# Kernel optimization log

Hardware: AMD Instinct MI355X
Metric: run time of the kernel (lower is better)

## Reference

```python
import jax, jax.numpy as jnp
import numpy as np

N_USERS = 4096
N_ITEMS = 4096
D = 64
L = 2
B = 4096
N = N_USERS + N_ITEMS


def setup_inputs() -> dict:
    key = jax.random.key(0)
    ks = jax.random.split(key, 24)
    g = lambda i, shape: jax.random.normal(ks[i], shape, dtype=jnp.float32) * 0.05
    # sparse-ish 0/1 adjacency (module calls adj.to_dense(); ~16 neighbors/node)
    adj = (jax.random.uniform(ks[0], (N, N), dtype=jnp.float32) < 0.002).astype(jnp.float32)
    users = jax.random.randint(ks[1], (B,), 0, N_USERS)
    pos_items = jax.random.randint(ks[2], (B,), 0, N_ITEMS)
    neg_items = jax.random.randint(ks[3], (B,), 0, N_ITEMS)
    return {
        "adj_matrix": adj,
        "users": users,
        "pos_items": pos_items,
        "neg_items": neg_items,
        "user_table": g(4, (N_USERS, D)),
        "item_table": g(5, (N_ITEMS, D)),
        "gcn_W": g(6, (L, D, D)), "gcn_b": g(7, (L, D)),
        "gat_W": g(8, (L, D, D)), "gat_b": g(9, (L, D)),
        "attn_W": g(10, (L, 2 * D)), "attn_b": g(11, (L,)),
        "fuse_W": g(12, (L, 2 * D, D)), "fuse_b": g(13, (L, D)),
        "actor_W": g(14, (D, D)), "actor_b": g(15, (D,)),
        "critic_W1": g(16, (2 * D, D)), "critic_b1": g(17, (D,)),
        "critic_W2": g(18, (D, 1)), "critic_b2": g(19, (1,)),
        "layer_weights": jnp.ones((L,), dtype=jnp.float32),
    }


def _leaky(x):
    return jnp.where(x >= 0, x, 0.01 * x)  # F.leaky_relu default slope


def reference(adj_matrix, users, pos_items, neg_items, user_table, item_table,
              gcn_W, gcn_b, gat_W, gat_b, attn_W, attn_b, fuse_W, fuse_b,
              actor_W, actor_b, critic_W1, critic_b1, critic_W2, critic_b2,
              layer_weights):
    all_emb = jnp.concatenate([user_table, item_table], axis=0)  # [N, D]

    # GCN stack: spmm(adj, x) then linear, relu
    gcn = [all_emb]
    for l in range(L):
        h = adj_matrix @ gcn[-1]
        gcn.append(jax.nn.relu(h @ gcn_W[l] + gcn_b[l]))

    # GAT stack: e[i,j] = leaky_relu(a1.h_i + a2.h_j + b); multiply-mask by adj, row softmax
    gat = [all_emb]
    for l in range(L):
        h = gat[-1] @ gat_W[l] + gat_b[l]  # [N, D]
        a1, a2 = attn_W[l, :D], attn_W[l, D:]
        e = _leaky((h @ a1)[:, None] + (h @ a2)[None, :] + attn_b[l])  # [N, N]
        attn = jax.nn.softmax(e * adj_matrix, axis=1)  # faithful: multiply-mask, not -inf
        gat.append(jax.nn.relu(attn @ h))

    lw = jax.nn.softmax(layer_weights)
    fused = jnp.zeros((N, D), dtype=all_emb.dtype)
    for i in range(L):
        cat = jnp.concatenate([gcn[i + 1], gat[i + 1]], axis=1)  # [N, 2D]
        fused = fused + lw[i] * jax.nn.relu(cat @ fuse_W[i] + fuse_b[i])

    user_emb, item_emb = fused[:N_USERS], fused[N_USERS:]
    u = user_emb[users]
    p = item_emb[pos_items]
    n = item_emb[neg_items]

    uf = u @ actor_W + actor_b  # Actor
    pos_score = jnp.sum(uf * p, axis=1)
    neg_score = jnp.sum(uf * n, axis=1)

    def critic(a, b):
        x = jnp.concatenate([a, b], axis=1)
        hidden = jax.nn.relu(x @ critic_W1 + critic_b1)
        return hidden @ critic_W2 + critic_b2

    return pos_score, neg_score, critic(u, p), critic(u, n)
```

## Files before the change

kernel.cpp:

```cpp
#include <hip/hip_runtime.h>

#define NTOT 8192
#define NU 4096
#define D 64
#define MAXN 128

__device__ __forceinline__ float wave_sum(float x){
  #pragma unroll
  for(int off=32;off;off>>=1) x += __shfl_xor(x,off);
  return x;
}
__device__ __forceinline__ float wave_max(float x){
  #pragma unroll
  for(int off=32;off;off>>=1) x = fmaxf(x,__shfl_xor(x,off));
  return x;
}

__global__ __launch_bounds__(256) void build_ell(const float* __restrict__ adj,
                                                 int* __restrict__ ell,
                                                 int* __restrict__ nnz){
  int lane = threadIdx.x & 63;
  int row  = blockIdx.x * 4 + (threadIdx.x >> 6);
  const float4* arow = (const float4*)(adj + (size_t)row * NTOT);
  int base = 0;
  for(int c0 = 0; c0 < NTOT/4; c0 += 64){
    float4 v = arow[c0 + lane];
    #pragma unroll
    for(int j = 0; j < 4; ++j){
      float f = (j==0)?v.x:(j==1)?v.y:(j==2)?v.z:v.w;
      unsigned long long m = __ballot(f != 0.0f);
      if(f != 0.0f){
        int slot = base + __popcll(m & ((1ull<<lane)-1ull));
        if(slot < MAXN) ell[row*MAXN + slot] = (c0 + lane)*4 + j;
      }
      base += __popcll(m);
    }
  }
  if(lane == 0) nnz[row] = base > MAXN ? MAXN : base;
}

__global__ void concat_emb(const float* __restrict__ ut, const float* __restrict__ it,
                           float* __restrict__ all_emb){
  int i = blockIdx.x * 256 + threadIdx.x;
  all_emb[i] = (i < NU*D) ? ut[i] : it[i - NU*D];
}

__global__ __launch_bounds__(256) void gcn_layer(const float* __restrict__ x,
    const int* __restrict__ ell, const int* __restrict__ nnz,
    const float* __restrict__ W, const float* __restrict__ b,
    float* __restrict__ y){
  __shared__ float Ws[D*D];
  __shared__ float bs[D];
  for(int i = threadIdx.x; i < D*D; i += 256) Ws[i] = W[i];
  if(threadIdx.x < D) bs[threadIdx.x] = b[threadIdx.x];
  __syncthreads();
  int lane = threadIdx.x & 63;
  int row  = blockIdx.x * 4 + (threadIdx.x >> 6);
  int cnt  = nnz[row];
  const int* cols = ell + row*MAXN;
  float acc = 0.f;
  for(int t = 0; t < cnt; ++t){
    int j = cols[t];
    acc += x[j*D + lane];
  }
  float yd = bs[lane];
  #pragma unroll 8
  for(int k = 0; k < D; ++k) yd += __shfl(acc, k) * Ws[k*D + lane];
  y[row*D + lane] = fmaxf(yd, 0.f);
}

__global__ __launch_bounds__(256) void gat_h(const float* __restrict__ x,
    const float* __restrict__ W, const float* __restrict__ b,
    const float* __restrict__ aW,
    float* __restrict__ h, float* __restrict__ qv, float* __restrict__ kvv){
  __shared__ float Ws[D*D];
  __shared__ float bs[D], a1s[D], a2s[D];
  for(int i = threadIdx.x; i < D*D; i += 256) Ws[i] = W[i];
  if(threadIdx.x < D){
    bs[threadIdx.x]  = b[threadIdx.x];
    a1s[threadIdx.x] = aW[threadIdx.x];
    a2s[threadIdx.x] = aW[D + threadIdx.x];
  }
  __syncthreads();
  int lane = threadIdx.x & 63;
  int row  = blockIdx.x * 4 + (threadIdx.x >> 6);
  float xd = x[row*D + lane];
  float hd = bs[lane];
  #pragma unroll 8
  for(int k = 0; k < D; ++k) hd += __shfl(xd, k) * Ws[k*D + lane];
  h[row*D + lane] = hd;
  float q  = wave_sum(hd * a1s[lane]);
  float kk = wave_sum(hd * a2s[lane]);
  if(lane == 0){ qv[row] = q; kvv[row] = kk; }
}

__global__ void colsum_part(const float* __restrict__ h, float* __restrict__ part){
  int d = threadIdx.x;
  int b = blockIdx.x;
  float s = 0.f;
  for(int r = b*32; r < b*32 + 32; ++r) s += h[r*D + d];
  part[b*D + d] = s;
}
__global__ void colsum_final(const float* __restrict__ part, float* __restrict__ S){
  int d = threadIdx.x;
  float s = 0.f;
  for(int b = 0; b < 256; ++b) s += part[b*D + d];
  S[d] = s;
}

__global__ __launch_bounds__(256) void gat_attn(const float* __restrict__ h,
    const float* __restrict__ qv, const float* __restrict__ kvv,
    const int* __restrict__ ell, const int* __restrict__ nnz,
    const float* __restrict__ S, const float* __restrict__ attn_b_p,
    float* __restrict__ out){
  int lane = threadIdx.x & 63;
  int row  = blockIdx.x * 4 + (threadIdx.x >> 6);
  int cnt  = nnz[row];
  float q  = qv[row];
  float ab = attn_b_p[0];
  const int* cols = ell + row*MAXN;
  float m = 0.f;
  for(int t0 = 0; t0 < cnt; t0 += 64){
    int t = t0 + lane;
    float e = -1e30f;
    if(t < cnt){
      float x = q + kvv[cols[t]] + ab;
      e = (x >= 0.f) ? x : 0.01f * x;
    }
    m = fmaxf(m, wave_max(e));
  }
  float em = expf(-m);
  float Z  = (float)(NTOT - cnt) * em;
  float accd = 0.f, hsumd = 0.f;
  for(int t0 = 0; t0 < cnt; t0 += 64){
    int t = t0 + lane;
    float w = 0.f; int col = 0;
    if(t < cnt){
      col = cols[t];
      float x = q + kvv[col] + ab;
      float e = (x >= 0.f) ? x : 0.01f * x;
      w = expf(e - m);
    }
    Z += wave_sum(w);
    int lim = (cnt - t0 < 64) ? (cnt - t0) : 64;
    for(int tt = 0; tt < lim; ++tt){
      float wt = __shfl(w, tt);
      int  j   = __shfl(col, tt);
      float hv = h[j*D + lane];
      accd  += wt * hv;
      hsumd += hv;
    }
  }
  float outd = (accd + em * (S[lane] - hsumd)) / Z;
  out[row*D + lane] = fmaxf(outd, 0.f);
}

__global__ __launch_bounds__(256) void fuse_kernel(const float* __restrict__ gcn1,
    const float* __restrict__ gat1, const float* __restrict__ gcn2, const float* __restrict__ gat2,
    const float* __restrict__ fuse_W, const float* __restrict__ fuse_b,
    const float* __restrict__ layer_w, float* __restrict__ fused){
  __shared__ float Wf[2*D*D];
  __shared__ float bf_[D];
  int lane = threadIdx.x & 63;
  int row  = blockIdx.x * 4 + (threadIdx.x >> 6);
  float l0 = layer_w[0], l1 = layer_w[1];
  float mx = fmaxf(l0, l1);
  float e0 = expf(l0-mx), e1 = expf(l1-mx);
  float inv = 1.f/(e0+e1);
  float lw0 = e0*inv, lw1 = e1*inv;

  for(int i = threadIdx.x; i < 2*D*D; i += 256) Wf[i] = fuse_W[i];
  if(threadIdx.x < D) bf_[threadIdx.x] = fuse_b[threadIdx.x];
  __syncthreads();
  float g = gcn1[row*D + lane], a = gat1[row*D + lane];
  float y0 = bf_[lane];
  #pragma unroll 8
  for(int k = 0; k < D; ++k){
    y0 += __shfl(g, k) * Wf[k*D + lane];
    y0 += __shfl(a, k) * Wf[(D+k)*D + lane];
  }
  __syncthreads();
  for(int i = threadIdx.x; i < 2*D*D; i += 256) Wf[i] = fuse_W[2*D*D + i];
  if(threadIdx.x < D) bf_[threadIdx.x] = fuse_b[D + threadIdx.x];
  __syncthreads();
  g = gcn2[row*D + lane]; a = gat2[row*D + lane];
  float y1 = bf_[lane];
  #pragma unroll 8
  for(int k = 0; k < D; ++k){
    y1 += __shfl(g, k) * Wf[k*D + lane];
    y1 += __shfl(a, k) * Wf[(D+k)*D + lane];
  }
  fused[row*D + lane] = lw0*fmaxf(y0,0.f) + lw1*fmaxf(y1,0.f);
}

__global__ __launch_bounds__(256) void score_kernel(const float* __restrict__ fused,
    const int* __restrict__ users, const int* __restrict__ pos, const int* __restrict__ neg,
    const float* __restrict__ AW, const float* __restrict__ abias,
    const float* __restrict__ cW1, const float* __restrict__ cb1,
    const float* __restrict__ cW2, const float* __restrict__ cb2,
    float* __restrict__ out){
  __shared__ float AWs[D*D];
  __shared__ float C1s[2*D*D];
  __shared__ float abs_[D], cb1s[D], C2s[D];
  for(int i = threadIdx.x; i < D*D; i += 256) AWs[i] = AW[i];
  for(int i = threadIdx.x; i < 2*D*D; i += 256) C1s[i] = cW1[i];
  if(threadIdx.x < D){
    abs_[threadIdx.x] = abias[threadIdx.x];
    cb1s[threadIdx.x] = cb1[threadIdx.x];
    C2s[threadIdx.x]  = cW2[threadIdx.x];
  }
  __syncthreads();
  int lane = threadIdx.x & 63;
  int bi   = blockIdx.x * 4 + (threadIdx.x >> 6);
  int ui = users[bi], pi = pos[bi] + NU, ni = neg[bi] + NU;
  float ud = fused[ui*D + lane], pd = fused[pi*D + lane], nd = fused[ni*D + lane];
  float ufd = abs_[lane];
  #pragma unroll 8
  for(int k = 0; k < D; ++k) ufd += __shfl(ud, k) * AWs[k*D + lane];
  float ps = wave_sum(ufd * pd);
  float ns = wave_sum(ufd * nd);
  float hu = cb1s[lane];
  #pragma unroll 8
  for(int k = 0; k < D; ++k) hu += __shfl(ud, k) * C1s[k*D + lane];
  float hp = hu, hn = hu;
  #pragma unroll 8
  for(int k = 0; k < D; ++k){
    float pk = __shfl(pd, k), nk = __shfl(nd, k);
    hp += pk * C1s[(D+k)*D + lane];
    hn += nk * C1s[(D+k)*D + lane];
  }
  hp = fmaxf(hp, 0.f); hn = fmaxf(hn, 0.f);
  float cp = wave_sum(hp * C2s[lane]);
  float cn = wave_sum(hn * C2s[lane]);
  if(lane == 0){
    out[bi]          = ps;
    out[4096  + bi]  = ns;
    out[8192  + bi]  = cp + cb2[0];
    out[12288 + bi]  = cn + cb2[0];
  }
}

extern "C" void kernel_launch(void* const* d_in, const int* in_sizes, int n_in,
                              void* d_out, int out_size, void* d_ws, size_t ws_size,
                              hipStream_t stream){
  const float* adj        = (const float*)d_in[0];
  const int*   users      = (const int*)d_in[1];
  const int*   pos        = (const int*)d_in[2];
  const int*   neg        = (const int*)d_in[3];
  const float* user_table = (const float*)d_in[4];
  const float* item_table = (const float*)d_in[5];
  const float* gcn_W      = (const float*)d_in[6];
  const float* gcn_b      = (const float*)d_in[7];
  const float* gat_W      = (const float*)d_in[8];
  const float* gat_b      = (const float*)d_in[9];
  const float* attn_W     = (const float*)d_in[10];
  const float* attn_b     = (const float*)d_in[11];
  const float* fuse_W     = (const float*)d_in[12];
  const float* fuse_b     = (const float*)d_in[13];
  const float* actor_W    = (const float*)d_in[14];
  const float* actor_b    = (const float*)d_in[15];
  const float* cW1        = (const float*)d_in[16];
  const float* cb1        = (const float*)d_in[17];
  const float* cW2        = (const float*)d_in[18];
  const float* cb2        = (const float*)d_in[19];
  const float* layer_w    = (const float*)d_in[20];

  const int ND = NTOT * D;
  float* ws      = (float*)d_ws;
  float* all_emb = ws;
  float* gcn1    = all_emb + ND;
  float* gcn2    = gcn1 + ND;
  float* gat1    = gcn2 + ND;
  float* gat2    = gat1 + ND;
  float* hbuf    = gat2 + ND;
  float* fusedb  = hbuf + ND;
  float* qv      = fusedb + ND;
  float* kv      = qv + NTOT;
  float* Spart   = kv + NTOT;
  float* Svec    = Spart + 256*D;
  int*   nnz     = (int*)(Svec + D);
  int*   ell     = nnz + NTOT;

  build_ell<<<NTOT/4, 256, 0, stream>>>(adj, ell, nnz);
  concat_emb<<<ND/256, 256, 0, stream>>>(user_table, item_table, all_emb);

  gcn_layer<<<NTOT/4, 256, 0, stream>>>(all_emb, ell, nnz, gcn_W,        gcn_b,     gcn1);
  gcn_layer<<<NTOT/4, 256, 0, stream>>>(gcn1,    ell, nnz, gcn_W + D*D,  gcn_b + D, gcn2);

  gat_h<<<NTOT/4, 256, 0, stream>>>(all_emb, gat_W, gat_b, attn_W, hbuf, qv, kv);
  colsum_part<<<256, 64, 0, stream>>>(hbuf, Spart);
  colsum_final<<<1, 64, 0, stream>>>(Spart, Svec);
  gat_attn<<<NTOT/4, 256, 0, stream>>>(hbuf, qv, kv, ell, nnz, Svec, attn_b, gat1);

  gat_h<<<NTOT/4, 256, 0, stream>>>(gat1, gat_W + D*D, gat_b + D, attn_W + 2*D, hbuf, qv, kv);
  colsum_part<<<256, 64, 0, stream>>>(hbuf, Spart);
  colsum_final<<<1, 64, 0, stream>>>(Spart, Svec);
  gat_attn<<<NTOT/4, 256, 0, stream>>>(hbuf, qv, kv, ell, nnz, Svec, attn_b + 1, gat2);

  fuse_kernel<<<NTOT/4, 256, 0, stream>>>(gcn1, gat1, gcn2, gat2, fuse_W, fuse_b, layer_w, fusedb);
  score_kernel<<<4096/4, 256, 0, stream>>>(fusedb, users, pos, neg,
                                           actor_W, actor_b, cW1, cb1, cW2, cb2,
                                           (float*)d_out);
}
```

Before: 210.0 us.

## Fuse pipeline into five multi-role kernels with padded ELL and atomic column sums

Replaces the roughly fourteen launches with five kernels. Independent stages share one launch by splitting the grid on block index: ELL build with concat, GCN layer with GAT projection, and GCN layer 2 with GAT attention 1, the first fuse half and the GAT layer 2 projection. The two-pass column sum becomes per-block atomicAdds. The ELL width drops to 64 and is padded with a sentinel index that points at a zero row, so gathers can be unrolled by 8 without bounds checks. Shuffles are replaced with readlane broadcasts, and all-zero float4 chunks are skipped in the adjacency scan. The gains come from fewer launches and sync points, and the cost is a dependence on every row having at most 64 neighbours, plus float atomic ordering nondeterminism.

Measured after the change: 221.1 us. 5.3% more time.

```diff
diff --git a/kernel.cpp b/kernel.cpp
--- a/kernel.cpp
+++ b/kernel.cpp
@@ -1,199 +1,256 @@
 #include <hip/hip_runtime.h>
 
 #define NTOT 8192
+#define NROW 2048
 #define NU 4096
 #define D 64
-#define MAXN 128
-
-__device__ __forceinline__ float wave_sum(float x){
+#define MAXN 64
+#define ND (NTOT*D)
+
+__device__ __forceinline__ float wsum(float x){
   #pragma unroll
-  for(int off=32;off;off>>=1) x += __shfl_xor(x,off);
+  for(int o=32;o;o>>=1) x += __shfl_xor(x,o);
   return x;
 }
-__device__ __forceinline__ float wave_max(float x){
+__device__ __forceinline__ float wmax(float x){
   #pragma unroll
-  for(int off=32;off;off>>=1) x = fmaxf(x,__shfl_xor(x,off));
+  for(int o=32;o;o>>=1) x = fmaxf(x,__shfl_xor(x,o));
   return x;
 }
-
-__global__ __launch_bounds__(256) void build_ell(const float* __restrict__ adj,
-                                                 int* __restrict__ ell,
-                                                 int* __restrict__ nnz){
-  int lane = threadIdx.x & 63;
-  int row  = blockIdx.x * 4 + (threadIdx.x >> 6);
-  const float4* arow = (const float4*)(adj + (size_t)row * NTOT);
-  int base = 0;
-  for(int c0 = 0; c0 < NTOT/4; c0 += 64){
-    float4 v = arow[c0 + lane];
-    #pragma unroll
-    for(int j = 0; j < 4; ++j){
-      float f = (j==0)?v.x:(j==1)?v.y:(j==2)?v.z:v.w;
-      unsigned long long m = __ballot(f != 0.0f);
-      if(f != 0.0f){
-        int slot = base + __popcll(m & ((1ull<<lane)-1ull));
-        if(slot < MAXN) ell[row*MAXN + slot] = (c0 + lane)*4 + j;
+__device__ __forceinline__ float bcastf(float x, int k){
+  return __uint_as_float(__builtin_amdgcn_readlane(__float_as_uint(x), (unsigned)k));
+}
+__device__ __forceinline__ int bcasti(int x, int k){
+  return (int)__builtin_amdgcn_readlane((unsigned)x, (unsigned)k);
+}
+
+__device__ __forceinline__ float gat_attn_row(const float* __restrict__ h,
+    const float* __restrict__ kvv, const float* __restrict__ S,
+    const int* __restrict__ cols, int cnt, float q, float ab, int lane){
+  int t = lane;
+  int col = (t < cnt) ? cols[t] : 0;
+  float e = -1e30f;
+  if(t < cnt){
+    float xx = q + kvv[col] + ab;
+    e = (xx >= 0.f) ? xx : 0.01f * xx;
+  }
+  float m  = fmaxf(0.f, wmax(e));
+  float w  = (t < cnt) ? expf(e - m) : 0.f;
+  float em = expf(-m);
+  float Z  = (float)(NTOT - cnt) * em + wsum(w);
+  float acc = 0.f, hsum = 0.f;
+  for(int tt = 0; tt < cnt; ++tt){
+    float wt = bcastf(w, tt);
+    int   jc = bcasti(col, tt);
+    float hv = h[jc*D + lane];
+    acc  = fmaf(wt, hv, acc);
+    hsum += hv;
+  }
+  float outv = (acc + em * (S[lane] - hsum)) / Z;
+  return fmaxf(outv, 0.f);
+}
+
+__global__ __launch_bounds__(256) void kA(const float* __restrict__ adj,
+    const float* __restrict__ ut, const float* __restrict__ it,
+    float* __restrict__ all_emb, int* __restrict__ ell, int* __restrict__ nnz,
+    float* __restrict__ Svec0, float* __restrict__ Svec1, float* __restrict__ gcn1){
+  int bid = blockIdx.x, tid = threadIdx.x;
+  if(bid < NROW){
+    int lane = tid & 63;
+    int row  = bid*4 + (tid >> 6);
+    ell[row*MAXN + lane] = NTOT;
+    const float4* arow = (const float4*)(adj + (size_t)row * NTOT);
+    int base = 0;
+    for(int c0 = 0; c0 < NTOT/4; c0 += 64){
+      float4 v = arow[c0 + lane];
+      int nib = (v.x!=0.f?1:0) | (v.y!=0.f?2:0) | (v.z!=0.f?4:0) | (v.w!=0.f?8:0);
+      if(__ballot(nib != 0) == 0ull) continue;
+      #pragma unroll
+      for(int j = 0; j < 4; ++j){
+        unsigned long long m = __ballot(((nib>>j)&1) != 0);
+        if(m){
+          if((nib>>j)&1){
+            int below = __builtin_amdgcn_mbcnt_hi((unsigned)(m>>32),
+                        __builtin_amdgcn_mbcnt_lo((unsigned)m, 0u));
+            int slot = base + below;
+            if(slot < MAXN) ell[row*MAXN + slot] = (c0 + lane)*4 + j;
+          }
+          base += __popcll(m);
+        }
       }
-      base += __popcll(m);
-    }
-  }
-  if(lane == 0) nnz[row] = base > MAXN ? MAXN : base;
-}
-
-__global__ void concat_emb(const float* __restrict__ ut, const float* __restrict__ it,
-                           float* __restrict__ all_emb){
-  int i = blockIdx.x * 256 + threadIdx.x;
-  all_emb[i] = (i < NU*D) ? ut[i] : it[i - NU*D];
-}
-
-__global__ __launch_bounds__(256) void gcn_layer(const float* __restrict__ x,
+    }
+    if(lane == 0) nnz[row] = base > MAXN ? MAXN : base;
+  } else if(bid < 2*NROW){
+    int i = (bid - NROW)*256 + tid;
+    all_emb[i] = (i < NU*D) ? ut[i] : it[i - NU*D];
+  } else {
+    if(tid < D){
+      Svec0[tid] = 0.f; Svec1[tid] = 0.f;
+      all_emb[ND + tid] = 0.f;
+      gcn1[ND + tid]    = 0.f;
+    }
+  }
+}
+
+__global__ __launch_bounds__(256) void kB(const float* __restrict__ all_emb,
     const int* __restrict__ ell, const int* __restrict__ nnz,
-    const float* __restrict__ W, const float* __restrict__ b,
-    float* __restrict__ y){
+    const float* __restrict__ gcn_W, const float* __restrict__ gcn_b,
+    const float* __restrict__ gat_W, const float* __restrict__ gat_b,
+    const float* __restrict__ attn_W,
+    float* __restrict__ gcn1, float* __restrict__ h0,
+    float* __restrict__ qv0, float* __restrict__ kv0, float* __restrict__ Svec0){
   __shared__ float Ws[D*D];
-  __shared__ float bs[D];
-  for(int i = threadIdx.x; i < D*D; i += 256) Ws[i] = W[i];
-  if(threadIdx.x < D) bs[threadIdx.x] = b[threadIdx.x];
-  __syncthreads();
-  int lane = threadIdx.x & 63;
-  int row  = blockIdx.x * 4 + (threadIdx.x >> 6);
-  int cnt  = nnz[row];
+  __shared__ float red[4][D];
+  int tid = threadIdx.x, lane = tid & 63, wid = tid >> 6;
+  int bid = blockIdx.x;
+  if(bid < NROW){
+    for(int i = tid; i < D*D; i += 256) Ws[i] = gcn_W[i];
+    __syncthreads();
+    int row = bid*4 + wid;
+    int cnt = nnz[row];
+    const int* cols = ell + row*MAXN;
+    float acc = 0.f;
+    int cnt8 = (cnt + 7) & ~7;
+    for(int t = 0; t < cnt8; t += 8){
+      #pragma unroll
+      for(int u = 0; u < 8; ++u){
+        int j = cols[t + u];
+        acc += all_emb[j*D + lane];
+      }
+    }
+    float y = gcn_b[lane];
+    #pragma unroll 16
+    for(int k = 0; k < D; ++k) y = fmaf(bcastf(acc, k), Ws[k*D + lane], y);
+    gcn1[row*D + lane] = fmaxf(y, 0.f);
+  } else {
+    for(int i = tid; i < D*D; i += 256) Ws[i] = gat_W[i];
+    __syncthreads();
+    int row = (bid - NROW)*4 + wid;
+    float xr = all_emb[row*D + lane];
+    float h = gat_b[lane];
+    #pragma unroll 16
+    for(int k = 0; k < D; ++k) h = fmaf(bcastf(xr, k), Ws[k*D + lane], h);
+    h0[row*D + lane] = h;
+    float q  = wsum(h * attn_W[lane]);
+    float kk = wsum(h * attn_W[D + lane]);
+    if(lane == 0){ qv0[row] = q; kv0[row] = kk; }
+    red[wid][lane] = h;
+    __syncthreads();
+    if(wid == 0){
+      float s = red[0][lane] + red[1][lane] + red[2][lane] + red[3][lane];
+      atomicAdd(&Svec0[lane], s);
+    }
+  }
+}
+
+__global__ __launch_bounds__(256) void kC(
+    const float* __restrict__ all_emb, const int* __restrict__ ell, const int* __restrict__ nnz,
+    const float* __restrict__ gcn1, const float* __restrict__ h0,
+    const float* __restrict__ qv0, const float* __restrict__ kv0, const float* __restrict__ Svec0,
+    const float* __restrict__ gcn_W, const float* __restrict__ gcn_b,
+    const float* __restrict__ gat_W, const float* __restrict__ gat_b,
+    const float* __restrict__ attn_W, const float* __restrict__ attn_b,
+    const float* __restrict__ fuse_W, const float* __restrict__ fuse_b,
+    const float* __restrict__ layer_w,
+    float* __restrict__ gcn2, float* __restrict__ h1,
+    float* __restrict__ qv1, float* __restrict__ kv1, float* __restrict__ Svec1,
+    float* __restrict__ fusedb){
+  __shared__ float Ws[D*D];
+  __shared__ float red[4][D];
+  int tid = threadIdx.x, lane = tid & 63, wid = tid >> 6;
+  int bid = blockIdx.x;
+  if(bid < NROW){
+    for(int i = tid; i < D*D; i += 256) Ws[i] = gcn_W[D*D + i];
+    __syncthreads();
+    int row = bid*4 + wid;
+    int cnt = nnz[row];
+    const int* cols = ell + row*MAXN;
+    float acc = 0.f;
+    int cnt8 = (cnt + 7) & ~7;
+    for(int t = 0; t < cnt8; t += 8){
+      #pragma unroll
+      for(int u = 0; u < 8; ++u){
+        int j = cols[t + u];
+        acc += gcn1[j*D + lane];
+      }
+    }
+    float y = gcn_b[D + lane];
+    #pragma unroll 16
+    for(int k = 0; k < D; ++k) y = fmaf(bcastf(acc, k), Ws[k*D + lane], y);
+    gcn2[row*D + lane] = fmaxf(y, 0.f);
+  } else {
+    int row = (bid - NROW)*4 + wid;
+    int cnt = nnz[row];
+    const int* cols = ell + row*MAXN;
+    float g1 = gat_attn_row(h0, kv0, Svec0, cols, cnt, qv0[row], attn_b[0], lane);
+    float gc1 = gcn1[row*D + lane];
+    float l0 = layer_w[0], l1 = layer_w[1];
+    float mx = fmaxf(l0, l1);
+    float e0 = expf(l0 - mx), e1 = expf(l1 - mx);
+    float lw0 = e0 / (e0 + e1);
+    for(int i = tid; i < D*D; i += 256) Ws[i] = fuse_W[i];
+    __syncthreads();
+    float y = fuse_b[lane];
+    #pragma unroll 16
+    for(int k = 0; k < D; ++k) y = fmaf(bcastf(gc1, k), Ws[k*D + lane], y);
+    __syncthreads();
+    for(int i = tid; i < D*D; i += 256) Ws[i] = fuse_W[D*D + i];
+    __syncthreads();
+    #pragma unroll 16
+    for(int k = 0; k < D; ++k) y = fmaf(bcastf(g1, k), Ws[k*D + lane], y);
+    fusedb[row*D + lane] = lw0 * fmaxf(y, 0.f);
+    __syncthreads();
+    for(int i = tid; i < D*D; i += 256) Ws[i] = gat_W[D*D + i];
+    __syncthreads();
+    float h = gat_b[D + lane];
+    #pragma unroll 16
+    for(int k = 0; k < D; ++k) h = fmaf(bcastf(g1, k), Ws[k*D + lane], h);
+    h1[row*D + lane] = h;
+    float qq = wsum(h * attn_W[2*D + lane]);
+    float kk = wsum(h * attn_W[3*D + lane]);
+    if(lane == 0){ qv1[row] = qq; kv1[row] = kk; }
+    red[wid][lane] = h;
+    __syncthreads();
+    if(wid == 0){
+      float s = red[0][lane] + red[1][lane] + red[2][lane] + red[3][lane];
+      atomicAdd(&Svec1[lane], s);
+    }
+  }
+}
+
+__global__ __launch_bounds__(256) void kE(
+    const int* __restrict__ ell, const int* __restrict__ nnz,
+    const float* __restrict__ gcn2, const float* __restrict__ h1,
+    const float* __restrict__ qv1, const float* __restrict__ kv1, const float* __restrict__ Svec1,
+    const float* __restrict__ attn_b,
+    const float* __restrict__ fuse_W, const float* __restrict__ fuse_b,
+    const float* __restrict__ layer_w,
+    float* __restrict__ fusedb){
+  __shared__ float Ws[D*D];
+  int tid = threadIdx.x, lane = tid & 63, wid = tid >> 6;
+  int row = blockIdx.x*4 + wid;
+  int cnt = nnz[row];
   const int* cols = ell + row*MAXN;
-  float acc = 0.f;
-  for(int t = 0; t < cnt; ++t){
-    int j = cols[t];
-    acc += x[j*D + lane];
-  }
-  float yd = bs[lane];
-  #pragma unroll 8
-  for(int k = 0; k < D; ++k) yd += __shfl(acc, k) * Ws[k*D + lane];
-  y[row*D + lane] = fmaxf(yd, 0.f);
-}
-
-__global__ __launch_bounds__(256) void gat_h(const float* __restrict__ x,
-    const float* __restrict__ W, const float* __restrict__ b,
-    const float* __restrict__ aW,
-    float* __restrict__ h, float* __restrict__ qv, float* __restrict__ kvv){
-  __shared__ float Ws[D*D];
-  __shared__ float bs[D], a1s[D], a2s[D];
-  for(int i = threadIdx.x; i < D*D; i += 256) Ws[i] = W[i];
-  if(threadIdx.x < D){
-    bs[threadIdx.x]  = b[threadIdx.x];
-    a1s[threadIdx.x] = aW[threadIdx.x];
-    a2s[threadIdx.x] = aW[D + threadIdx.x];
-  }
-  __syncthreads();
-  int lane = threadIdx.x & 63;
-  int row  = blockIdx.x * 4 + (threadIdx.x >> 6);
-  float xd = x[row*D + lane];
-  float hd = bs[lane];
-  #pragma unroll 8
-  for(int k = 0; k < D; ++k) hd += __shfl(xd, k) * Ws[k*D + lane];
-  h[row*D + lane] = hd;
-  float q  = wave_sum(hd * a1s[lane]);
-  float kk = wave_sum(hd * a2s[lane]);
-  if(lane == 0){ qv[row] = q; kvv[row] = kk; }
-}
-
-__global__ void colsum_part(const float* __restrict__ h, float* __restrict__ part){
-  int d = threadIdx.x;
-  int b = blockIdx.x;
-  float s = 0.f;
-  for(int r = b*32; r < b*32 + 32; ++r) s += h[r*D + d];
-  part[b*D + d] = s;
-}
-__global__ void colsum_final(const float* __restrict__ part, float* __restrict__ S){
-  int d = threadIdx.x;
-  float s = 0.f;
-  for(int b = 0; b < 256; ++b) s += part[b*D + d];
-  S[d] = s;
-}
-
-__global__ __launch_bounds__(256) void gat_attn(const float* __restrict__ h,
-    const float* __restrict__ qv, const float* __restrict__ kvv,
-    const int* __restrict__ ell, const int* __restrict__ nnz,
-    const float* __restrict__ S, const float* __restrict__ attn_b_p,
-    float* __restrict__ out){
-  int lane = threadIdx.x & 63;
-  int row  = blockIdx.x * 4 + (threadIdx.x >> 6);
-  int cnt  = nnz[row];
-  float q  = qv[row];
-  float ab = attn_b_p[0];
-  const int* cols = ell + row*MAXN;
-  float m = 0.f;
-  for(int t0 = 0; t0 < cnt; t0 += 64){
-    int t = t0 + lane;
-    float e = -1e30f;
-    if(t < cnt){
-      float x = q + kvv[cols[t]] + ab;
-      e = (x >= 0.f) ? x : 0.01f * x;
-    }
-    m = fmaxf(m, wave_max(e));
-  }
-  float em = expf(-m);
-  float Z  = (float)(NTOT - cnt) * em;
-  float accd = 0.f, hsumd = 0.f;
-  for(int t0 = 0; t0 < cnt; t0 += 64){
-    int t = t0 + lane;
-    float w = 0.f; int col = 0;
-    if(t < cnt){
-      col = cols[t];
-      float x = q + kvv[col] + ab;
-      float e = (x >= 0.f) ? x : 0.01f * x;
-      w = expf(e - m);
-    }
-    Z += wave_sum(w);
-    int lim = (cnt - t0 < 64) ? (cnt - t0) : 64;
-    for(int tt = 0; tt < lim; ++tt){
-      float wt = __shfl(w, tt);
-      int  j   = __shfl(col, tt);
-      float hv = h[j*D + lane];
-      accd  += wt * hv;
-      hsumd += hv;
-    }
-  }
-  float outd = (accd + em * (S[lane] - hsumd)) / Z;
-  out[row*D + lane] = fmaxf(outd, 0.f);
-}
-
-__global__ __launch_bounds__(256) void fuse_kernel(const float* __restrict__ gcn1,
-    const float* __restrict__ gat1, const float* __restrict__ gcn2, const float* __restrict__ gat2,
-    const float* __restrict__ fuse_W, const float* __restrict__ fuse_b,
-    const float* __restrict__ layer_w, float* __restrict__ fused){
-  __shared__ float Wf[2*D*D];
-  __shared__ float bf_[D];
-  int lane = threadIdx.x & 63;
-  int row  = blockIdx.x * 4 + (threadIdx.x >> 6);
+  float g2 = gat_attn_row(h1, kv1, Svec1, cols, cnt, qv1[row], attn_b[1], lane);
+  float gc2 = gcn2[row*D + lane];
   float l0 = layer_w[0], l1 = layer_w[1];
   float mx = fmaxf(l0, l1);
-  float e0 = expf(l0-mx), e1 = expf(l1-mx);
-  float inv = 1.f/(e0+e1);
-  float lw0 = e0*inv, lw1 = e1*inv;
-
-  for(int i = threadIdx.x; i < 2*D*D; i += 256) Wf[i] = fuse_W[i];
-  if(threadIdx.x < D) bf_[threadIdx.x] = fuse_b[threadIdx.x];
+  float e0 = expf(l0 - mx), e1 = expf(l1 - mx);
+  float lw1 = e1 / (e0 + e1);
+  for(int i = tid; i < D*D; i += 256) Ws[i] = fuse_W[2*D*D + i];
   __syncthreads();
-  float g = gcn1[row*D + lane], a = gat1[row*D + lane];
-  float y0 = bf_[lane];
-  #pragma unroll 8
-  for(int k = 0; k < D; ++k){
-    y0 += __shfl(g, k) * Wf[k*D + lane];
-    y0 += __shfl(a, k) * Wf[(D+k)*D + lane];
-  }
+  float y = fuse_b[D + lane];
+  #pragma unroll 16
+  for(int k = 0; k < D; ++k) y = fmaf(bcastf(gc2, k), Ws[k*D + lane], y);
   __syncthreads();
-  for(int i = threadIdx.x; i < 2*D*D; i += 256) Wf[i] = fuse_W[2*D*D + i];
-  if(threadIdx.x < D) bf_[threadIdx.x] = fuse_b[D + threadIdx.x];
+  for(int i = tid; i < D*D; i += 256) Ws[i] = fuse_W[3*D*D + i];
   __syncthreads();
-  g = gcn2[row*D + lane]; a = gat2[row*D + lane];
-  float y1 = bf_[lane];
-  #pragma unroll 8
-  for(int k = 0; k < D; ++k){
-    y1 += __shfl(g, k) * Wf[k*D + lane];
-    y1 += __shfl(a, k) * Wf[(D+k)*D + lane];
-  }
-  fused[row*D + lane] = lw0*fmaxf(y0,0.f) + lw1*fmaxf(y1,0.f);
-}
-
-__global__ __launch_bounds__(256) void score_kernel(const float* __restrict__ fused,
+  #pragma unroll 16
+  for(int k = 0; k < D; ++k) y = fmaf(bcastf(g2, k), Ws[k*D + lane], y);
+  fusedb[row*D + lane] += lw1 * fmaxf(y, 0.f);
+}
+
+__global__ __launch_bounds__(256) void kF(const float* __restrict__ fused,
     const int* __restrict__ users, const int* __restrict__ pos, const int* __restrict__ neg,
     const float* __restrict__ AW, const float* __restrict__ abias,
     const float* __restrict__ cW1, const float* __restrict__ cb1,
@@ -202,41 +259,42 @@
   __shared__ float AWs[D*D];
   __shared__ float C1s[2*D*D];
   __shared__ float abs_[D], cb1s[D], C2s[D];
-  for(int i = threadIdx.x; i < D*D; i += 256) AWs[i] = AW[i];
-  for(int i = threadIdx.x; i < 2*D*D; i += 256) C1s[i] = cW1[i];
-  if(threadIdx.x < D){
-    abs_[threadIdx.x] = abias[threadIdx.x];
-    cb1s[threadIdx.x] = cb1[threadIdx.x];
-    C2s[threadIdx.x]  = cW2[threadIdx.x];
+  int tid = threadIdx.x;
+  for(int i = tid; i < D*D; i += 256) AWs[i] = AW[i];
+  for(int i = tid; i < 2*D*D; i += 256) C1s[i] = cW1[i];
+  if(tid < D){
+    abs_[tid] = abias[tid];
+    cb1s[tid] = cb1[tid];
+    C2s[tid]  = cW2[tid];
   }
   __syncthreads();
-  int lane = threadIdx.x & 63;
-  int bi   = blockIdx.x * 4 + (threadIdx.x >> 6);
+  int lane = tid & 63;
+  int bi   = blockIdx.x*4 + (tid >> 6);
   int ui = users[bi], pi = pos[bi] + NU, ni = neg[bi] + NU;
   float ud = fused[ui*D + lane], pd = fused[pi*D + lane], nd = fused[ni*D + lane];
   float ufd = abs_[lane];
-  #pragma unroll 8
-  for(int k = 0; k < D; ++k) ufd += __shfl(ud, k) * AWs[k*D + lane];
-  float ps = wave_sum(ufd * pd);
-  float ns = wave_sum(ufd * nd);
+  #pragma unroll 16
+  for(int k = 0; k < D; ++k) ufd = fmaf(bcastf(ud, k), AWs[k*D + lane], ufd);
+  float ps = wsum(ufd * pd);
+  float ns = wsum(ufd * nd);
   float hu = cb1s[lane];
-  #pragma unroll 8
-  for(int k = 0; k < D; ++k) hu += __shfl(ud, k) * C1s[k*D + lane];
+  #pragma unroll 16
+  for(int k = 0; k < D; ++k) hu = fmaf(bcastf(ud, k), C1s[k*D + lane], hu);
   float hp = hu, hn = hu;
-  #pragma unroll 8
+  #pragma unroll 16
   for(int k = 0; k < D; ++k){
-    float pk = __shfl(pd, k), nk = __shfl(nd, k);
-    hp += pk * C1s[(D+k)*D + lane];
-    hn += nk * C1s[(D+k)*D + lane];
+    float pk = bcastf(pd, k), nk = bcastf(nd, k);
+    hp = fmaf(pk, C1s[(D+k)*D + lane], hp);
+    hn = fmaf(nk, C1s[(D+k)*D + lane], hn);
   }
   hp = fmaxf(hp, 0.f); hn = fmaxf(hn, 0.f);
-  float cp = wave_sum(hp * C2s[lane]);
-  float cn = wave_sum(hn * C2s[lane]);
+  float cp = wsum(hp * C2s[lane]);
+  float cn = wsum(hn * C2s[lane]);
   if(lane == 0){
-    out[bi]          = ps;
-    out[4096  + bi]  = ns;
-    out[8192  + bi]  = cp + cb2[0];
-    out[12288 + bi]  = cn + cb2[0];
+    out[bi]         = ps;
+    out[4096  + bi] = ns;
+    out[8192  + bi] = cp + cb2[0];
+    out[12288 + bi] = cn + cb2[0];
   }
 }
 
@@ -265,40 +323,32 @@
   const float* cb2        = (const float*)d_in[19];
   const float* layer_w    = (const float*)d_in[20];
 
-  const int ND = NTOT * D;
   float* ws      = (float*)d_ws;
   float* all_emb = ws;
-  float* gcn1    = all_emb + ND;
-  float* gcn2    = gcn1 + ND;
-  float* gat1    = gcn2 + ND;
-  float* gat2    = gat1 + ND;
-  float* hbuf    = gat2 + ND;
-  float* fusedb  = hbuf + ND;
-  float* qv      = fusedb + ND;
-  float* kv      = qv + NTOT;
-  float* Spart   = kv + NTOT;
-  float* Svec    = Spart + 256*D;
-  int*   nnz     = (int*)(Svec + D);
+  float* gcn1    = all_emb + ND + D;
+  float* gcn2    = gcn1 + ND + D;
+  float* h0      = gcn2 + ND;
+  float* h1      = h0 + ND;
+  float* fusedb  = h1 + ND;
+  float* qv0     = fusedb + ND;
+  float* kv0     = qv0 + NTOT;
+  float* qv1     = kv0 + NTOT;
+  float* kv1     = qv1 + NTOT;
+  float* Svec0   = kv1 + NTOT;
+  float* Svec1   = Svec0 + D;
+  int*   nnz     = (int*)(Svec1 + D);
   int*   ell     = nnz + NTOT;
 
-  build_ell<<<NTOT/4, 256, 0, stream>>>(adj, ell, nnz);
-  concat_emb<<<ND/256, 256, 0, stream>>>(user_table, item_table, all_emb);
-
-  gcn_layer<<<NTOT/4, 256, 0, stream>>>(all_emb, ell, nnz, gcn_W,        gcn_b,     gcn1);
-  gcn_layer<<<NTOT/4, 256, 0, stream>>>(gcn1,    ell, nnz, gcn_W + D*D,  gcn_b + D, gcn2);
-
-  gat_h<<<NTOT/4, 256, 0, stream>>>(all_emb, gat_W, gat_b, attn_W, hbuf, qv, kv);
-  colsum_part<<<256, 64, 0, stream>>>(hbuf, Spart);
-  colsum_final<<<1, 64, 0, stream>>>(Spart, Svec);
-  gat_attn<<<NTOT/4, 256, 0, stream>>>(hbuf, qv, kv, ell, nnz, Svec, attn_b, gat1);
-
-  gat_h<<<NTOT/4, 256, 0, stream>>>(gat1, gat_W + D*D, gat_b + D, attn_W + 2*D, hbuf, qv, kv);
-  colsum_part<<<256, 64, 0, stream>>>(hbuf, Spart);
-  colsum_final<<<1, 64, 0, stream>>>(Spart, Svec);
-  gat_attn<<<NTOT/4, 256, 0, stream>>>(hbuf, qv, kv, ell, nnz, Svec, attn_b + 1, gat2);
-
-  fuse_kernel<<<NTOT/4, 256, 0, stream>>>(gcn1, gat1, gcn2, gat2, fuse_W, fuse_b, layer_w, fusedb);
-  score_kernel<<<4096/4, 256, 0, stream>>>(fusedb, users, pos, neg,
-                                           actor_W, actor_b, cW1, cb1, cW2, cb2,
-                                           (float*)d_out);
-}
+  kA<<<2*NROW + 1, 256, 0, stream>>>(adj, user_table, item_table,
+                                     all_emb, ell, nnz, Svec0, Svec1, gcn1);
+  kB<<<2*NROW, 256, 0, stream>>>(all_emb, ell, nnz, gcn_W, gcn_b, gat_W, gat_b,
+                                 attn_W, gcn1, h0, qv0, kv0, Svec0);
+  kC<<<2*NROW, 256, 0, stream>>>(all_emb, ell, nnz, gcn1, h0, qv0, kv0, Svec0,
+                                 gcn_W, gcn_b, gat_W, gat_b, attn_W, attn_b,
+                                 fuse_W, fuse_b, layer_w,
+                                 gcn2, h1, qv1, kv1, Svec1, fusedb);
+  kE<<<NROW, 256, 0, stream>>>(ell, nnz, gcn2, h1, qv1, kv1, Svec1, attn_b,
+                               fuse_W, fuse_b, layer_w, fusedb);
+  kF<<<1024, 256, 0, stream>>>(fusedb, users, pos, neg, actor_W, actor_b,
+                               cW1, cb1, cW2, cb2, (float*)d_out);
+}
```
